# Kernel optimization log

Measured on AMD Instinct MI355X. Metric: run time of the kernel, lower is better.

Reference implementation:

```python
import jax, jax.numpy as jnp
import numpy as np

B, H, W, C, HEADS = 4, 64, 64, 512, 8
HD = C // HEADS
L = H * W
BIAS_LEVEL = 0.1
LN_EPS = 1e-5


def _ln(x, g, b):
    mu = jnp.mean(x, axis=-1, keepdims=True)
    var = jnp.var(x, axis=-1, keepdims=True)
    return (x - mu) * jax.lax.rsqrt(var + LN_EPS) * g + b


def setup_inputs() -> dict:
    key = jax.random.key(0)
    ks = jax.random.split(key, 16)
    s = 0.02
    return {
        "x": jax.random.normal(ks[0], (B, L, C), jnp.float32),
        "rpe": jax.random.normal(ks[1], (H, HEADS, W, W), jnp.float32),
        "qkv_w": jax.random.normal(ks[2], (3 * C, C), jnp.float32) * s,
        "proj_w": jax.random.normal(ks[3], (C, C), jnp.float32) * s,
        "proj_b": jnp.zeros((C,), jnp.float32),
        "norm1_w": jnp.ones((C,), jnp.float32),
        "norm1_b": jnp.zeros((C,), jnp.float32),
        "norm2_w": jnp.ones((C,), jnp.float32),
        "norm2_b": jnp.zeros((C,), jnp.float32),
        "fc1_w": jax.random.normal(ks[4], (4 * C, C), jnp.float32) * s,
        "fc1_b": jnp.zeros((4 * C,), jnp.float32),
        "fc2_w": jax.random.normal(ks[5], (C, 4 * C), jnp.float32) * s,
        "fc2_b": jnp.zeros((C,), jnp.float32),
    }


def reference(x, rpe, qkv_w, proj_w, proj_b, norm1_w, norm1_b, norm2_w, norm2_b,
              fc1_w, fc1_b, fc2_w, fc2_b):
    # --- qkv projection ---
    img = _ln(x, norm1_w, norm1_b)
    qkv = (img @ qkv_w.T).reshape(B, L, 3, C)
    q, k, v = qkv[:, :, 0], qkv[:, :, 1], qkv[:, :, 2]

    # idx=0 horizontal windows: each row of the HxW grid is a window of len W.
    def to_win(t):  # (B, L, C) -> (B*H, heads, W, hd)
        return t.reshape(B * H, W, HEADS, HD).transpose(0, 2, 1, 3)

    qw, kw, vw = to_win(q), to_win(k), to_win(v)

    # attention scores + relative position bias (RPE tiled over batch)
    attn = jnp.einsum('whqd,whkd->whqk', qw, kw)
    attn = attn + BIAS_LEVEL * jnp.tile(rpe, (B, 1, 1, 1))

    # magnitude gate M per window
    M = jnp.mean(jnp.abs(attn), axis=(1, 2, 3), keepdims=True)  # (B*H,1,1,1)
    M = M / jnp.max(M)
    M = jnp.maximum(M, 0.5)

    # cosine-based score transform: 1 - cos(pi/2 * l2normalize(attn))
    nrm = jnp.maximum(jnp.linalg.norm(attn, axis=-1, keepdims=True), 1e-12)
    attn = 1.0 - jnp.cos((attn / nrm) * (jnp.pi / 2.0))
    attn = attn * M

    o = jnp.einsum('whqk,whkd->whqd', attn, vw)  # (B*H, heads, W, hd)
    o = o.transpose(0, 2, 1, 3).reshape(B, L, C)

    # residual gating by (1 - M)
    res = (x.reshape(B * H, 1, W, C) * (1.0 - M)).reshape(B, L, C)
    attened = o + res

    attened = attened @ proj_w.T + proj_b
    x1 = x + attened

    h = _ln(x1, norm2_w, norm2_b)
    h = jax.nn.gelu(h @ fc1_w.T + fc1_b, approximate=False)
    h = h @ fc2_w.T + fc2_b
    return x1 + h
```

## Files before the change

kernel.cpp:

```cpp
#include <hip/hip_runtime.h>
#include <hip/hip_bf16.h>
#include <math.h>

typedef unsigned short u16;
typedef __bf16 bf16x8 __attribute__((ext_vector_type(8)));
typedef float f32x4 __attribute__((ext_vector_type(4)));
typedef unsigned short u16x8 __attribute__((ext_vector_type(8)));

typedef const __attribute__((address_space(1))) void* gas_ptr;
typedef __attribute__((address_space(3))) void* las_ptr;

__device__ __forceinline__ float bf2f(u16 u) {
    union { unsigned int i; float f; } x;
    x.i = ((unsigned int)u) << 16;
    return x.f;
}
__device__ __forceinline__ u16 f2bf(float f) {
    __hip_bfloat16 h = __float2bfloat16(f);
    return __builtin_bit_cast(u16, h);
}
__device__ __forceinline__ __bf16 f2bfr(float f) {
    __hip_bfloat16 h = __float2bfloat16(f);
    return __builtin_bit_cast(__bf16, h);
}
__device__ __forceinline__ void load_lds16(const void* g, void* l) {
    __builtin_amdgcn_global_load_lds((gas_ptr)g, (las_ptr)l, 16, 0, 0);
}
__device__ __forceinline__ float gelu_f(float v) {
    const float a = fabsf(v) * 0.70710678118654752f;
    const float tt = 1.0f / fmaf(0.3275911f, a, 1.0f);
    float poly = fmaf(tt, 1.061405429f, -1.453152027f);
    poly = fmaf(tt, poly, 1.421413741f);
    poly = fmaf(tt, poly, -0.284496736f);
    poly = fmaf(tt, poly, 0.254829592f);
    const float erfa = 1.0f - poly * tt * __expf(-a * a);
    const float erfv = copysignf(erfa, v);
    return 0.5f * v * (1.0f + erfv);
}

__global__ __launch_bounds__(256) void cvt_all_k(const float* __restrict__ qkv_w,
                                                 const float* __restrict__ proj_w,
                                                 const float* __restrict__ fc1w,
                                                 const float* __restrict__ fc2w,
                                                 u16* __restrict__ wqkv,
                                                 u16* __restrict__ wproj,
                                                 u16* __restrict__ wfc1,
                                                 u16* __restrict__ wfc2) {
    const int b = blockIdx.x;
    const float* src; u16* dst; int off;
    if (b < 768)       { src = qkv_w;  dst = wqkv;  off = b; }
    else if (b < 1024) { src = proj_w; dst = wproj; off = b - 768; }
    else if (b < 2048) { src = fc1w;   dst = wfc1;  off = b - 1024; }
    else               { src = fc2w;   dst = wfc2;  off = b - 2048; }
    const int i = off * 256 + threadIdx.x;
    const float4 v = ((const float4*)src)[i];
    ushort4 o;
    o.x = f2bf(v.x); o.y = f2bf(v.y); o.z = f2bf(v.z); o.w = f2bf(v.w);
    ((ushort4*)dst)[i] = o;
}

__global__ __launch_bounds__(256) void ln_row_k(const float* __restrict__ x,
                                                const float* __restrict__ gw,
                                                const float* __restrict__ gb,
                                                u16* __restrict__ outp) {
    const int row = blockIdx.x * 4 + (threadIdx.x >> 6);
    const int lane = threadIdx.x & 63;
    const float* rp = x + (size_t)row * 512 + lane * 8;
    const float4 a = *(const float4*)rp;
    const float4 b = *(const float4*)(rp + 4);
    float s = a.x + a.y + a.z + a.w + b.x + b.y + b.z + b.w;
    float q = a.x*a.x + a.y*a.y + a.z*a.z + a.w*a.w
            + b.x*b.x + b.y*b.y + b.z*b.z + b.w*b.w;
    #pragma unroll
    for (int o = 1; o < 64; o <<= 1) {
        s += __shfl_xor(s, o);
        q += __shfl_xor(q, o);
    }
    const float mean = s * (1.0f / 512.0f);
    const float var = q * (1.0f / 512.0f) - mean * mean;
    const float rstd = rsqrtf(var + 1e-5f);
    const float4 g0 = *(const float4*)(gw + lane * 8);
    const float4 g1 = *(const float4*)(gw + lane * 8 + 4);
    const float4 c0 = *(const float4*)(gb + lane * 8);
    const float4 c1 = *(const float4*)(gb + lane * 8 + 4);
    u16x8 o16;
    o16[0] = f2bf((a.x - mean) * rstd * g0.x + c0.x);
    o16[1] = f2bf((a.y - mean) * rstd * g0.y + c0.y);
    o16[2] = f2bf((a.z - mean) * rstd * g0.z + c0.z);
    o16[3] = f2bf((a.w - mean) * rstd * g0.w + c0.w);
    o16[4] = f2bf((b.x - mean) * rstd * g1.x + c1.x);
    o16[5] = f2bf((b.y - mean) * rstd * g1.y + c1.y);
    o16[6] = f2bf((b.z - mean) * rstd * g1.z + c1.z);
    o16[7] = f2bf((b.w - mean) * rstd * g1.w + c1.w);
    *(u16x8*)(outp + (size_t)row * 512 + lane * 8) = o16;
}

__global__ __launch_bounds__(256) void ln_row_bf_k(const u16* __restrict__ x1,
                                                   const float* __restrict__ gw,
                                                   const float* __restrict__ gb,
                                                   u16* __restrict__ outp) {
    const int row = blockIdx.x * 4 + (threadIdx.x >> 6);
    const int lane = threadIdx.x & 63;
    const u16x8 v = *(const u16x8*)(x1 + (size_t)row * 512 + lane * 8);
    float f[8];
    float s = 0.f, q = 0.f;
    #pragma unroll
    for (int e = 0; e < 8; ++e) {
        f[e] = bf2f(v[e]);
        s += f[e]; q += f[e] * f[e];
    }
    #pragma unroll
    for (int o = 1; o < 64; o <<= 1) {
        s += __shfl_xor(s, o);
        q += __shfl_xor(q, o);
    }
    const float mean = s * (1.0f / 512.0f);
    const float var = q * (1.0f / 512.0f) - mean * mean;
    const float rstd = rsqrtf(var + 1e-5f);
    const float4 g0 = *(const float4*)(gw + lane * 8);
    const float4 g1 = *(const float4*)(gw + lane * 8 + 4);
    const float4 c0 = *(const float4*)(gb + lane * 8);
    const float4 c1 = *(const float4*)(gb + lane * 8 + 4);
    u16x8 o16;
    o16[0] = f2bf((f[0] - mean) * rstd * g0.x + c0.x);
    o16[1] = f2bf((f[1] - mean) * rstd * g0.y + c0.y);
    o16[2] = f2bf((f[2] - mean) * rstd * g0.z + c0.z);
    o16[3] = f2bf((f[3] - mean) * rstd * g0.w + c0.w);
    o16[4] = f2bf((f[4] - mean) * rstd * g1.x + c1.x);
    o16[5] = f2bf((f[5] - mean) * rstd * g1.y + c1.y);
    o16[6] = f2bf((f[6] - mean) * rstd * g1.z + c1.z);
    o16[7] = f2bf((f[7] - mean) * rstd * g1.w + c1.w);
    *(u16x8*)(outp + (size_t)row * 512 + lane * 8) = o16;
}

template<int EPI, int AFUSE>
__global__ __launch_bounds__(256) void gemm_bt(const u16* __restrict__ A,
                                               const u16* __restrict__ W,
                                               const float* __restrict__ bias,
                                               const float* __restrict__ res_f,
                                               const u16* __restrict__ res_bf,
                                               void* __restrict__ outp,
                                               int M, int N, int K,
                                               const float* __restrict__ aM,
                                               const u16* __restrict__ aO,
                                               const float* __restrict__ aX) {
    __shared__ __bf16 As[2][128 * 64];
    __shared__ __bf16 Bs[2][128 * 64];
    const int t = threadIdx.x;
    const int l = t & 63;
    const int w = t >> 6;
    const int wm = w & 1, wn = w >> 1;
    const int bm = blockIdx.x * 128, bn = blockIdx.y * 128;
    const int r = l & 15, g4 = l >> 4;

    f32x4 acc[4][4] = {};

    const int rowS = t >> 3;
    const int cS = (t & 7) ^ (rowS & 7);
    const size_t rstep = (size_t)32 * K;
    const u16* wBase = W + (size_t)(bn + rowS) * K + cS * 8;
    const u16* aBase = A + (size_t)(bm + rowS) * K + cS * 8;
    const size_t afBase = (size_t)(bm + rowS) * K + cS * 8;

    float Mw[4];
    if (AFUSE == 1) {
        #pragma unroll
        for (int j = 0; j < 4; ++j) Mw[j] = aM[(bm + rowS + 32 * j) >> 6];
    }

    u16x8 ovr[4];
    float4 x0r[4], x1r[4];

    auto loadA = [&](int kt) __attribute__((always_inline)) {
        #pragma unroll
        for (int j = 0; j < 4; ++j) {
            const size_t gidx = afBase + j * rstep + kt;
            ovr[j] = *(const u16x8*)(aO + gidx);
            x0r[j] = *(const float4*)(aX + gidx);
            x1r[j] = *(const float4*)(aX + gidx + 4);
        }
    };
    auto writeA = [&](int buf) __attribute__((always_inline)) {
        #pragma unroll
        for (int j = 0; j < 4; ++j) {
            const float rf = 1.0f - Mw[j];
            bf16x8 val;
            val[0] = f2bfr(Mw[j] * bf2f(ovr[j][0]) + rf * x0r[j].x);
            val[1] = f2bfr(Mw[j] * bf2f(ovr[j][1]) + rf * x0r[j].y);
            val[2] = f2bfr(Mw[j] * bf2f(ovr[j][2]) + rf * x0r[j].z);
            val[3] = f2bfr(Mw[j] * bf2f(ovr[j][3]) + rf * x0r[j].w);
            val[4] = f2bfr(Mw[j] * bf2f(ovr[j][4]) + rf * x1r[j].x);
            val[5] = f2bfr(Mw[j] * bf2f(ovr[j][5]) + rf * x1r[j].y);
            val[6] = f2bfr(Mw[j] * bf2f(ovr[j][6]) + rf * x1r[j].z);
            val[7] = f2bfr(Mw[j] * bf2f(ovr[j][7]) + rf * x1r[j].w);
            *(bf16x8*)&As[buf][(j * 256 + t) * 8] = val;
        }
    };
    auto stageA_g = [&](int buf, int kt) __attribute__((always_inline)) {
        #pragma unroll
        for (int j = 0; j < 4; ++j)
            load_lds16(aBase + j * rstep + kt, &As[buf][(j * 256 + t) * 8]);
    };
    auto stageB = [&](int buf, int kt) __attribute__((always_inline)) {
        #pragma unroll
        for (int j = 0; j < 4; ++j)
            load_lds16(wBase + j * rstep + kt, &Bs[buf][(j * 256 + t) * 8]);
    };
    auto compute = [&](int buf) __attribute__((always_inline)) {
        bf16x8 af[4][2], bfr[4][2];
        #pragma unroll
        for (int i = 0; i < 4; ++i) {
            const int ra = wm * 64 + i * 16 + r;
            const int rb = wn * 64 + i * 16 + r;
            #pragma unroll
            for (int h = 0; h < 2; ++h) {
                af[i][h]  = *(const bf16x8*)&As[buf][ra * 64 + (((h * 4 + g4) ^ (ra & 7)) << 3)];
                bfr[i][h] = *(const bf16x8*)&Bs[buf][rb * 64 + (((h * 4 + g4) ^ (rb & 7)) << 3)];
            }
        }
        #pragma unroll
        for (int i = 0; i < 4; ++i)
            #pragma unroll
            for (int j = 0; j < 4; ++j)
                #pragma unroll
                for (int h = 0; h < 2; ++h)
                    acc[i][j] = __builtin_amdgcn_mfma_f32_16x16x32_bf16(
                        af[i][h], bfr[j][h], acc[i][j], 0, 0, 0);
    };

    const int nk = K >> 6;
    if (AFUSE == 1) { loadA(0); writeA(0); }
    else            stageA_g(0, 0);
    stageB(0, 0);
    __syncthreads();
    for (int s = 0; s < nk; ++s) {
        const int nb = (s + 1) & 1;
        if (s + 1 < nk) {
            if (AFUSE == 1) loadA((s + 1) << 6);
            else            stageA_g(nb, (s + 1) << 6);
            stageB(nb, (s + 1) << 6);
        }
        compute(s & 1);
        if (AFUSE == 1 && s + 1 < nk) writeA(nb);
        __syncthreads();
    }

    #pragma unroll
    for (int i = 0; i < 4; ++i) {
        #pragma unroll
        for (int j = 0; j < 4; ++j) {
            #pragma unroll
            for (int rr = 0; rr < 4; ++rr) {
                const int m = bm + wm * 64 + i * 16 + g4 * 4 + rr;
                const int n = bn + wn * 64 + j * 16 + r;
                float v = acc[i][j][rr];
                const size_t idx = (size_t)m * N + n;
                if (EPI == 0) {
                    ((u16*)outp)[idx] = f2bf(v);
                } else if (EPI == 1) {
                    ((u16*)outp)[idx] = f2bf(v + bias[n] + res_f[idx]);
                } else if (EPI == 2) {
                    ((u16*)outp)[idx] = f2bf(gelu_f(v + bias[n]));
                } else {
                    ((float*)outp)[idx] = v + bias[n] + bf2f(res_bf[idx]);
                }
            }
        }
    }
}

__global__ __launch_bounds__(256) void attn_k(const u16* __restrict__ qkv,
                                              const float* __restrict__ rpe,
                                              float* __restrict__ Mpart,
                                              u16* __restrict__ Obuf) {
    const int blk = blockIdx.x;
    const int wh = blk >> 3, head = blk & 7;
    const int himg = wh & 63;
    const int t = threadIdx.x, l = t & 63, w = t >> 6;
    __shared__ __bf16 Qs[4096];
    __shared__ __bf16 Ks[4096];
    __shared__ __bf16 Vt[4096];
    __shared__ __bf16 Ps[4096];
    __shared__ float red[4];

    #pragma unroll
    for (int p = 0; p < 2; ++p) {
        const int sb = (p * 256 + t) << 4;
        const int row = sb >> 7;
        const int gl = ((sb >> 4) & 7) ^ (row & 7);
        const size_t gsrc = (size_t)(wh * 64 + row) * 1536 + head * 64 + gl * 8;
        const int lbase = p * 2048 + w * 512;
        load_lds16(qkv + gsrc, &Qs[lbase]);
        load_lds16(qkv + gsrc + 512, &Ks[lbase]);
    }
    {
        const int k = t >> 2, dc = (t & 3) * 16;
        const u16* vr = qkv + (size_t)(wh * 64 + k) * 1536 + 1024 + head * 64 + dc;
        u16x8 v0 = *(const u16x8*)vr;
        u16x8 v1 = *(const u16x8*)(vr + 8);
        const int g = k >> 3, klo = k & 7;
        #pragma unroll
        for (int i = 0; i < 8; ++i) {
            const int d0 = dc + i, d1 = dc + 8 + i;
            Vt[d0 * 64 + ((g ^ (d0 & 7)) << 3) + klo] = __builtin_bit_cast(__bf16, (u16)v0[i]);
            Vt[d1 * 64 + ((g ^ (d1 & 7)) << 3) + klo] = __builtin_bit_cast(__bf16, (u16)v1[i]);
        }
    }
    __syncthreads();

    const int r = l & 15, g4 = l >> 4;
    f32x4 acc[4] = {};
    #pragma unroll
    for (int h = 0; h < 2; ++h) {
        const int rowq = w * 16 + r;
        bf16x8 aq = *(const bf16x8*)&Qs[rowq * 64 + (((h * 4 + g4) ^ (rowq & 7)) << 3)];
        #pragma unroll
        for (int j = 0; j < 4; ++j) {
            const int rowk = j * 16 + r;
            bf16x8 bk = *(const bf16x8*)&Ks[rowk * 64 + (((h * 4 + g4) ^ (rowk & 7)) << 3)];
            acc[j] = __builtin_amdgcn_mfma_f32_16x16x32_bf16(aq, bk, acc[j], 0, 0, 0);
        }
    }

    float v[4][4];
    float asum = 0.f;
    float ss[4] = {0.f, 0.f, 0.f, 0.f};
    const size_t rpe_base = (size_t)(himg * 8 + head) * 4096 + (size_t)(w * 16 + g4 * 4) * 64 + r;
    #pragma unroll
    for (int j = 0; j < 4; ++j) {
        #pragma unroll
        for (int rr = 0; rr < 4; ++rr) {
            const float val = acc[j][rr] + 0.1f * rpe[rpe_base + rr * 64 + j * 16];
            v[j][rr] = val;
            asum += fabsf(val);
            ss[rr] += val * val;
        }
    }
    #pragma unroll
    for (int m = 1; m < 16; m <<= 1) {
        #pragma unroll
        for (int rr = 0; rr < 4; ++rr) ss[rr] += __shfl_xor(ss[rr], m);
    }
    float srev[4];
    #pragma unroll
    for (int rr = 0; rr < 4; ++rr)
        srev[rr] = 0.25f / fmaxf(sqrtf(ss[rr]), 1e-12f);

    #pragma unroll
    for (int j = 0; j < 4; ++j) {
        #pragma unroll
        for (int rr = 0; rr < 4; ++rr) {
            const float pv = 1.0f - __builtin_amdgcn_cosf(v[j][rr] * srev[rr]);
            const int rl = g4 * 4 + rr;
            const int c = j * 16 + r;
            Ps[w * 1024 + rl * 64 + (((c >> 3) ^ (rl & 7)) << 3) + (c & 7)] = f2bfr(pv);
        }
    }

    f32x4 oacc[4] = {};
    #pragma unroll
    for (int ks = 0; ks < 2; ++ks) {
        const int ga = ks * 4 + g4;
        bf16x8 pa = *(const bf16x8*)&Ps[w * 1024 + r * 64 + ((ga ^ (r & 7)) << 3)];
        #pragma unroll
        for (int j = 0; j < 4; ++j) {
            const int d = j * 16 + r;
            bf16x8 vb = *(const bf16x8*)&Vt[d * 64 + ((ga ^ (d & 7)) << 3)];
            oacc[j] = __builtin_amdgcn_mfma_f32_16x16x32_bf16(pa, vb, oacc[j], 0, 0, 0);
        }
    }

    #pragma unroll
    for (int j = 0; j < 4; ++j) {
        #pragma unroll
        for (int rr = 0; rr < 4; ++rr) {
            const int token = wh * 64 + w * 16 + g4 * 4 + rr;
            Obuf[(size_t)token * 512 + head * 64 + j * 16 + r] = f2bf(oacc[j][rr]);
        }
    }

    #pragma unroll
    for (int o = 1; o < 64; o <<= 1) asum += __shfl_xor(asum, o);
    if (l == 0) red[w] = asum;
    __syncthreads();
    if (t == 0) Mpart[blk] = red[0] + red[1] + red[2] + red[3];
}

__global__ __launch_bounds__(256) void mfinal_k(const float* __restrict__ Mpart,
                                                float* __restrict__ M) {
    const int t = threadIdx.x;
    float m = 0.f;
    #pragma unroll
    for (int h = 0; h < 8; ++h) m += Mpart[t * 8 + h];
    m *= (1.0f / 32768.0f);
    float mx = m;
    #pragma unroll
    for (int o = 1; o < 64; o <<= 1) mx = fmaxf(mx, __shfl_xor(mx, o));
    __shared__ float red[4];
    if ((t & 63) == 0) red[t >> 6] = mx;
    __syncthreads();
    mx = fmaxf(fmaxf(red[0], red[1]), fmaxf(red[2], red[3]));
    M[t] = fmaxf(m / mx, 0.5f);
}

extern "C" void kernel_launch(void* const* d_in, const int* in_sizes, int n_in,
                              void* d_out, int out_size, void* d_ws, size_t ws_size,
                              hipStream_t stream) {
    (void)in_sizes; (void)n_in; (void)out_size; (void)ws_size;
    const float* x      = (const float*)d_in[0];
    const float* rpe    = (const float*)d_in[1];
    const float* qkv_w  = (const float*)d_in[2];
    const float* proj_w = (const float*)d_in[3];
    const float* proj_b = (const float*)d_in[4];
    const float* n1w    = (const float*)d_in[5];
    const float* n1b    = (const float*)d_in[6];
    const float* n2w    = (const float*)d_in[7];
    const float* n2b    = (const float*)d_in[8];
    const float* fc1w   = (const float*)d_in[9];
    const float* fc1b   = (const float*)d_in[10];
    const float* fc2w   = (const float*)d_in[11];
    const float* fc2b   = (const float*)d_in[12];
    float* out = (float*)d_out;

    char* ws = (char*)d_ws;
    float* Mpart = (float*)ws;
    float* Mbuf  = (float*)(ws + 8192);
    u16* wqkv  = (u16*)(ws + 16384);
    u16* wproj = (u16*)(ws + 16384 + 1572864);
    u16* wfc1  = (u16*)(ws + 16384 + 2097152);
    u16* wfc2  = (u16*)(ws + 16384 + 4194304);
    u16* bufA  = (u16*)(ws + 6307840);
    u16* bufB  = (u16*)(ws + 23085056);
    char* R    = ws + 39862272;
    u16*   qkvb = (u16*)R;
    u16*   Obuf = (u16*)(R + 50331648);
    u16*   gbuf = (u16*)R;

    cvt_all_k<<<3072, 256, 0, stream>>>(qkv_w, proj_w, fc1w, fc2w,
                                        wqkv, wproj, wfc1, wfc2);
    ln_row_k<<<4096, 256, 0, stream>>>(x, n1w, n1b, bufA);
    gemm_bt<0, 0><<<dim3(128, 12), 256, 0, stream>>>(
        bufA, wqkv, nullptr, nullptr, nullptr, qkvb, 16384, 1536, 512,
        nullptr, nullptr, nullptr);
    attn_k<<<2048, 256, 0, stream>>>(qkvb, rpe, Mpart, Obuf);
    mfinal_k<<<1, 256, 0, stream>>>(Mpart, Mbuf);
    gemm_bt<1, 1><<<dim3(128, 4), 256, 0, stream>>>(
        Obuf, wproj, proj_b, x, nullptr, bufA, 16384, 512, 512,
        Mbuf, Obuf, x);
    ln_row_bf_k<<<4096, 256, 0, stream>>>(bufA, n2w, n2b, bufB);
    gemm_bt<2, 0><<<dim3(128, 16), 256, 0, stream>>>(
        bufB, wfc1, fc1b, nullptr, nullptr, gbuf, 16384, 2048, 512,
        nullptr, nullptr, nullptr);
    gemm_bt<3, 0><<<dim3(128, 4), 256, 0, stream>>>(
        gbuf, wfc2, fc2b, nullptr, bufA, out, 16384, 512, 2048,
        nullptr, nullptr, nullptr);
}
```

Before: 205.1 us.

## Stage GEMM epilogue through LDS for vectorized coalesced stores

The GEMM epilogue now writes accumulators into a padded shared-memory tile, reusing the A/B staging buffers, and then has each thread emit 32 contiguous columns with 16-byte vector loads and stores for bias, residual and output. This replaces scattered 2- and 4-byte per-element global accesses. The fused A-operand path is also reorganized so the global loads, blend and LDS write happen together in the prefetch stage instead of being split around the MFMA compute. That removes the register-held prefetch but may expose global load latency before the compute, and the new epilogue adds extra barriers and LDS traffic.

```diff
diff --git a/kernel.cpp b/kernel.cpp
--- a/kernel.cpp
+++ b/kernel.cpp
@@ -144,8 +144,11 @@
                                                const float* __restrict__ aM,
                                                const u16* __restrict__ aO,
                                                const float* __restrict__ aX) {
-    __shared__ __bf16 As[2][128 * 64];
-    __shared__ __bf16 Bs[2][128 * 64];
+    __shared__ __align__(16) char smem[65536];
+    __bf16* Asm = (__bf16*)smem;
+    __bf16* Bsm = (__bf16*)(smem + 32768);
+    float*  EP  = (float*)smem;
+
     const int t = threadIdx.x;
     const int l = t & 63;
     const int w = t >> 6;
@@ -162,51 +165,41 @@
     const u16* aBase = A + (size_t)(bm + rowS) * K + cS * 8;
     const size_t afBase = (size_t)(bm + rowS) * K + cS * 8;
 
-    float Mw[4];
-    if (AFUSE == 1) {
-        #pragma unroll
-        for (int j = 0; j < 4; ++j) Mw[j] = aM[(bm + rowS + 32 * j) >> 6];
-    }
-
-    u16x8 ovr[4];
-    float4 x0r[4], x1r[4];
-
-    auto loadA = [&](int kt) __attribute__((always_inline)) {
+    auto stage = [&](int buf, int kt) {
         #pragma unroll
         for (int j = 0; j < 4; ++j) {
-            const size_t gidx = afBase + j * rstep + kt;
-            ovr[j] = *(const u16x8*)(aO + gidx);
-            x0r[j] = *(const float4*)(aX + gidx);
-            x1r[j] = *(const float4*)(aX + gidx + 4);
+            if (AFUSE == 1) {
+                const size_t gidx = afBase + j * rstep + kt;
+                const float Mw = aM[(bm + rowS + j * 32) >> 6];
+                const float rf = 1.0f - Mw;
+                const u16x8 ov = *(const u16x8*)(aO + gidx);
+                const float4 x0 = *(const float4*)(aX + gidx);
+                const float4 x1 = *(const float4*)(aX + gidx + 4);
+                bf16x8 val;
+                val[0] = f2bfr(Mw * bf2f(ov[0]) + rf * x0.x);
+                val[1] = f2bfr(Mw * bf2f(ov[1]) + rf * x0.y);
+                val[2] = f2bfr(Mw * bf2f(ov[2]) + rf * x0.z);
+                val[3] = f2bfr(Mw * bf2f(ov[3]) + rf * x0.w);
+                val[4] = f2bfr(Mw * bf2f(ov[4]) + rf * x1.x);
+                val[5] = f2bfr(Mw * bf2f(ov[5]) + rf * x1.y);
+                val[6] = f2bfr(Mw * bf2f(ov[6]) + rf * x1.z);
+                val[7] = f2bfr(Mw * bf2f(ov[7]) + rf * x1.w);
+                *(bf16x8*)&Asm[buf * 8192 + (j * 256 + t) * 8] = val;
+            } else {
+                load_lds16(aBase + j * rstep + kt,
+                           &Asm[buf * 8192 + (j * 256 + t) * 8]);
+            }
+            load_lds16(wBase + j * rstep + kt,
+                       &Bsm[buf * 8192 + (j * 256 + t) * 8]);
         }
     };
-    auto writeA = [&](int buf) __attribute__((always_inline)) {
-        #pragma unroll
-        for (int j = 0; j < 4; ++j) {
-            const float rf = 1.0f - Mw[j];
-            bf16x8 val;
-            val[0] = f2bfr(Mw[j] * bf2f(ovr[j][0]) + rf * x0r[j].x);
-            val[1] = f2bfr(Mw[j] * bf2f(ovr[j][1]) + rf * x0r[j].y);
-            val[2] = f2bfr(Mw[j] * bf2f(ovr[j][2]) + rf * x0r[j].z);
-            val[3] = f2bfr(Mw[j] * bf2f(ovr[j][3]) + rf * x0r[j].w);
-            val[4] = f2bfr(Mw[j] * bf2f(ovr[j][4]) + rf * x1r[j].x);
-            val[5] = f2bfr(Mw[j] * bf2f(ovr[j][5]) + rf * x1r[j].y);
-            val[6] = f2bfr(Mw[j] * bf2f(ovr[j][6]) + rf * x1r[j].z);
-            val[7] = f2bfr(Mw[j] * bf2f(ovr[j][7]) + rf * x1r[j].w);
-            *(bf16x8*)&As[buf][(j * 256 + t) * 8] = val;
-        }
-    };
-    auto stageA_g = [&](int buf, int kt) __attribute__((always_inline)) {
-        #pragma unroll
-        for (int j = 0; j < 4; ++j)
-            load_lds16(aBase + j * rstep + kt, &As[buf][(j * 256 + t) * 8]);
-    };
-    auto stageB = [&](int buf, int kt) __attribute__((always_inline)) {
-        #pragma unroll
-        for (int j = 0; j < 4; ++j)
-            load_lds16(wBase + j * rstep + kt, &Bs[buf][(j * 256 + t) * 8]);
-    };
-    auto compute = [&](int buf) __attribute__((always_inline)) {
+
+    const int nk = K >> 6;
+    stage(0, 0);
+    __syncthreads();
+    for (int s = 0; s < nk; ++s) {
+        if (s + 1 < nk) stage((s + 1) & 1, (s + 1) << 6);
+        const int buf = s & 1;
         bf16x8 af[4][2], bfr[4][2];
         #pragma unroll
         for (int i = 0; i < 4; ++i) {
@@ -214,8 +207,8 @@
             const int rb = wn * 64 + i * 16 + r;
             #pragma unroll
             for (int h = 0; h < 2; ++h) {
-                af[i][h]  = *(const bf16x8*)&As[buf][ra * 64 + (((h * 4 + g4) ^ (ra & 7)) << 3)];
-                bfr[i][h] = *(const bf16x8*)&Bs[buf][rb * 64 + (((h * 4 + g4) ^ (rb & 7)) << 3)];
+                af[i][h]  = *(const bf16x8*)&Asm[buf * 8192 + ra * 64 + (((h * 4 + g4) ^ (ra & 7)) << 3)];
+                bfr[i][h] = *(const bf16x8*)&Bsm[buf * 8192 + rb * 64 + (((h * 4 + g4) ^ (rb & 7)) << 3)];
             }
         }
         #pragma unroll
@@ -226,46 +219,81 @@
                 for (int h = 0; h < 2; ++h)
                     acc[i][j] = __builtin_amdgcn_mfma_f32_16x16x32_bf16(
                         af[i][h], bfr[j][h], acc[i][j], 0, 0, 0);
-    };
-
-    const int nk = K >> 6;
-    if (AFUSE == 1) { loadA(0); writeA(0); }
-    else            stageA_g(0, 0);
-    stageB(0, 0);
-    __syncthreads();
-    for (int s = 0; s < nk; ++s) {
-        const int nb = (s + 1) & 1;
-        if (s + 1 < nk) {
-            if (AFUSE == 1) loadA((s + 1) << 6);
-            else            stageA_g(nb, (s + 1) << 6);
-            stageB(nb, (s + 1) << 6);
-        }
-        compute(s & 1);
-        if (AFUSE == 1 && s + 1 < nk) writeA(nb);
         __syncthreads();
     }
 
-    #pragma unroll
-    for (int i = 0; i < 4; ++i) {
-        #pragma unroll
-        for (int j = 0; j < 4; ++j) {
-            #pragma unroll
-            for (int rr = 0; rr < 4; ++rr) {
-                const int m = bm + wm * 64 + i * 16 + g4 * 4 + rr;
-                const int n = bn + wn * 64 + j * 16 + r;
-                float v = acc[i][j][rr];
-                const size_t idx = (size_t)m * N + n;
-                if (EPI == 0) {
-                    ((u16*)outp)[idx] = f2bf(v);
-                } else if (EPI == 1) {
-                    ((u16*)outp)[idx] = f2bf(v + bias[n] + res_f[idx]);
-                } else if (EPI == 2) {
-                    ((u16*)outp)[idx] = f2bf(gelu_f(v + bias[n]));
-                } else {
-                    ((float*)outp)[idx] = v + bias[n] + bf2f(res_bf[idx]);
+    const int erow = t & 63;
+    const int cb   = (t >> 6) * 32;
+    float bias32[32];
+    if (EPI != 0) {
+        #pragma unroll
+        for (int k4 = 0; k4 < 8; ++k4)
+            *(float4*)&bias32[k4 * 4] = *(const float4*)(bias + bn + cb + k4 * 4);
+    }
+
+    #pragma unroll
+    for (int half = 0; half < 2; ++half) {
+        #pragma unroll
+        for (int ii = 0; ii < 2; ++ii) {
+            const int i = half * 2 + ii;
+            #pragma unroll
+            for (int j = 0; j < 4; ++j) {
+                #pragma unroll
+                for (int rr = 0; rr < 4; ++rr) {
+                    const int rl = wm * 32 + ii * 16 + g4 * 4 + rr;
+                    EP[rl * 129 + wn * 64 + j * 16 + r] = acc[i][j][rr];
                 }
             }
         }
+        __syncthreads();
+        const int m = bm + (erow >> 5) * 64 + (half * 2 + ((erow >> 4) & 1)) * 16 + (erow & 15);
+        float vals[32];
+        #pragma unroll
+        for (int k = 0; k < 32; ++k) vals[k] = EP[erow * 129 + cb + k];
+        const size_t obase = (size_t)m * N + bn + cb;
+        if (EPI == 0) {
+            u16x8 ov[4];
+            #pragma unroll
+            for (int k = 0; k < 32; ++k) ov[k >> 3][k & 7] = f2bf(vals[k]);
+            #pragma unroll
+            for (int k8 = 0; k8 < 4; ++k8)
+                *(u16x8*)((u16*)outp + obase + k8 * 8) = ov[k8];
+        } else if (EPI == 1) {
+            float rv[32];
+            #pragma unroll
+            for (int k4 = 0; k4 < 8; ++k4)
+                *(float4*)&rv[k4 * 4] = *(const float4*)(res_f + obase + k4 * 4);
+            u16x8 ov[4];
+            #pragma unroll
+            for (int k = 0; k < 32; ++k)
+                ov[k >> 3][k & 7] = f2bf(vals[k] + bias32[k] + rv[k]);
+            #pragma unroll
+            for (int k8 = 0; k8 < 4; ++k8)
+                *(u16x8*)((u16*)outp + obase + k8 * 8) = ov[k8];
+        } else if (EPI == 2) {
+            u16x8 ov[4];
+            #pragma unroll
+            for (int k = 0; k < 32; ++k)
+                ov[k >> 3][k & 7] = f2bf(gelu_f(vals[k] + bias32[k]));
+            #pragma unroll
+            for (int k8 = 0; k8 < 4; ++k8)
+                *(u16x8*)((u16*)outp + obase + k8 * 8) = ov[k8];
+        } else {
+            u16x8 rv[4];
+            #pragma unroll
+            for (int k8 = 0; k8 < 4; ++k8)
+                rv[k8] = *(const u16x8*)(res_bf + obase + k8 * 8);
+            #pragma unroll
+            for (int k4 = 0; k4 < 8; ++k4) {
+                float4 o4;
+                o4.x = vals[k4 * 4]     + bias32[k4 * 4]     + bf2f(rv[k4 >> 1][(k4 & 1) * 4]);
+                o4.y = vals[k4 * 4 + 1] + bias32[k4 * 4 + 1] + bf2f(rv[k4 >> 1][(k4 & 1) * 4 + 1]);
+                o4.z = vals[k4 * 4 + 2] + bias32[k4 * 4 + 2] + bf2f(rv[k4 >> 1][(k4 & 1) * 4 + 2]);
+                o4.w = vals[k4 * 4 + 3] + bias32[k4 * 4 + 3] + bf2f(rv[k4 >> 1][(k4 & 1) * 4 + 3]);
+                *(float4*)((float*)outp + obase + k4 * 4) = o4;
+            }
+        }
+        __syncthreads();
     }
 }
 
```

Result: slower. 211.7 us (+3.2%).
